# Kernel optimization log

Measured on AMD Instinct MI355X. Metric: run time of the kernel, lower is better.

The kernel has to match this reference:

```python
import jax, jax.numpy as jnp
from jax import lax
import numpy as np

B = 8192
NUM_CTX = 300; NUM_STN = 300; NUM_GPE = 20; NUM_GPI = 2; NUM_OUT = 20
FF_DIM = 20; FF_STEPS = 20; STN_ITERS = 50
ETA_GPE = 1.0; ETA_STN = 1.0 / 3.0; ETA_GPI = 0.1
A1 = 1.0; A2 = 1.0; THETAD1 = 0.0; THETAD2 = 0.0
UNITS = (64, 128, 64)

_SPECS = [("vf0", UNITS[0], NUM_CTX), ("vf1", UNITS[1], UNITS[0]), ("vf2", UNITS[2], UNITS[1]), ("vf3", 1, UNITS[2]),
          ("jd1", FF_DIM, NUM_CTX), ("jd2", FF_DIM, NUM_CTX), ("kd1", FF_DIM, NUM_CTX), ("kd2", FF_DIM, NUM_CTX),
          ("sg", NUM_GPE, NUM_STN), ("gs", NUM_STN, NUM_GPE), ("glat", NUM_GPE, NUM_GPE), ("slat", NUM_STN, NUM_STN),
          ("d1gpi", NUM_GPI, FF_DIM), ("stngpi", NUM_GPI, NUM_STN),
          ("ih", 4 * NUM_OUT, NUM_GPI), ("hh", 4 * NUM_OUT, NUM_OUT)]


def _lin_init(k, out_d, in_d):
    kw, kb = jax.random.split(k)
    bound = 1.0 / np.sqrt(in_d)
    w = jax.random.uniform(kw, (out_d, in_d), minval=-bound, maxval=bound, dtype=jnp.float32)
    b = jax.random.uniform(kb, (out_d,), minval=-bound, maxval=bound, dtype=jnp.float32)
    return w, b


def setup_inputs() -> dict:
    key = jax.random.key(0)
    ks = iter(jax.random.split(key, 40))
    inp = {}
    inp["stimulus"] = jax.random.normal(next(ks), (B, NUM_CTX), dtype=jnp.float32)
    inp["deltavf"] = jax.random.normal(next(ks), (B, 1), dtype=jnp.float32)
    inp["hx0"] = jax.random.uniform(next(ks), (B, NUM_OUT), dtype=jnp.float32)
    inp["cx0"] = jax.random.uniform(next(ks), (B, NUM_OUT), dtype=jnp.float32)
    for name, o, i in _SPECS:
        w, b = _lin_init(next(ks), o, i)
        inp["w_" + name] = w
        inp["b_" + name] = b
    return inp


def _lin(x, w, b):
    return x @ w.T + b


def _lstm_cell(x, h, c, w_ih, b_ih, w_hh, b_hh):
    gates = _lin(x, w_ih, b_ih) + _lin(h, w_hh, b_hh)
    i, f, g, o = jnp.split(gates, 4, axis=-1)  # torch LSTMCell gate order
    c_new = jax.nn.sigmoid(f) * c + jax.nn.sigmoid(i) * jnp.tanh(g)
    h_new = jax.nn.sigmoid(o) * jnp.tanh(c_new)
    return h_new, c_new


def reference(stimulus, deltavf, hx0, cx0,
              w_vf0, b_vf0, w_vf1, b_vf1, w_vf2, b_vf2, w_vf3, b_vf3,
              w_jd1, b_jd1, w_jd2, b_jd2, w_kd1, b_kd1, w_kd2, b_kd2,
              w_sg, b_sg, w_gs, b_gs, w_glat, b_glat, w_slat, b_slat,
              w_d1gpi, b_d1gpi, w_stngpi, b_stngpi,
              w_ih, b_ih, w_hh, b_hh):
    bsz = stimulus.shape[0]
    # value function head
    h = jax.nn.relu(_lin(stimulus, w_vf0, b_vf0))
    h = jax.nn.relu(_lin(h, w_vf1, b_vf1))
    h = jax.nn.relu(_lin(h, w_vf2, b_vf2))
    vt = jnp.tanh(_lin(h, w_vf3, b_vf3))  # [B, 1]

    lamd1 = jax.nn.sigmoid(A1 * (deltavf - THETAD1))  # [B, 1]
    lamd2 = jax.nn.sigmoid(A2 * (deltavf - THETAD2))  # [B, 1]

    # loop-invariant striatal drives (computed every iter in torch, same value)
    J_D1 = _lin(stimulus, w_jd1, b_jd1)
    J_D2 = _lin(stimulus, w_jd2, b_jd2)
    K_D1 = _lin(stimulus, w_kd1, b_kd1)
    K_D2 = _lin(stimulus, w_kd2, b_kd2)

    def ff_step(carry, _):
        v1, v2 = carry
        v1 = jax.nn.sigmoid(lamd1 * (J_D1 * (1.0 - v1) + (1.0 - K_D1) * v1))
        v2 = jax.nn.sigmoid(lamd2 * (J_D2 * (1.0 - v2) + (1.0 - K_D2) * v2))
        return (v1, v2), None

    z_ff = jnp.zeros((bsz, FF_DIM), dtype=stimulus.dtype)
    (V_D1, V_D2), _ = lax.scan(ff_step, (z_ff, z_ff), None, length=FF_STEPS)

    V_GPi_DP = _lin(V_D1, w_d1gpi, b_d1gpi)  # [B, num_gpi]

    def stn_step(carry, _):
        xgpe, xstn, vstn, vgpi, hx, cx = carry
        xgpe = xgpe + ETA_GPE * (-xgpe + _lin(vstn, w_sg, b_sg) + _lin(xgpe, w_glat, b_glat) - V_D2)
        xstn = xstn + ETA_STN * (-xstn + _lin(xgpe, w_gs, b_gs) + _lin(vstn, w_slat, b_slat))
        vstn = jnp.tanh(lamd2 * xstn)
        V_GPi_IP = lamd2 * _lin(vstn, w_stngpi, b_stngpi)
        vgpi = vgpi + ETA_GPI * (-vgpi - V_GPi_DP + 2.0 * V_GPi_IP)
        hx, cx = _lstm_cell(-vgpi, hx, cx, w_ih, b_ih, w_hh, b_hh)
        return (xgpe, xstn, vstn, vgpi, hx, cx), None

    carry0 = (jnp.zeros((bsz, NUM_GPE), dtype=stimulus.dtype),
              jnp.zeros((bsz, NUM_STN), dtype=stimulus.dtype),
              jnp.zeros((bsz, NUM_STN), dtype=stimulus.dtype),  # tanh(lamd2*0) = 0
              jnp.zeros((bsz, NUM_GPI), dtype=stimulus.dtype),
              hx0, cx0)
    carry, _ = lax.scan(stn_step, carry0, None, length=STN_ITERS)
    hx = carry[4]
    return hx, vt
```

## Files before the change

kernel.cpp:

```cpp
#include <hip/hip_runtime.h>


typedef _Float16 f16_t;
typedef _Float16 f16x8 __attribute__((ext_vector_type(8)));
typedef _Float16 f16x4 __attribute__((ext_vector_type(4)));
typedef float floatx4 __attribute__((ext_vector_type(4)));

#define BTOT 8192
#define BM   32
#define NTHR 512
#define NBLK 256
#define VSTR 328
#define XST  32

struct Params {
  const float *stimulus, *deltavf, *hx0, *cx0;
  const float *w_vf0, *b_vf0, *w_vf1, *b_vf1, *w_vf2, *b_vf2, *w_vf3, *b_vf3;
  const float *w_jd1, *b_jd1, *w_jd2, *b_jd2, *w_kd1, *b_kd1, *w_kd2, *b_kd2;
  const float *w_sg, *b_sg, *w_gs, *b_gs, *w_glat, *b_glat, *w_slat, *b_slat;
  const float *w_d1gpi, *b_d1gpi, *w_stngpi, *b_stngpi;
  const float *w_ih, *b_ih, *w_hh, *b_hh;
  float* out;
};

struct __align__(16) Smem {
  f16_t vstn[BM * VSTR];
  f16_t xgpe[2][BM * XST];
  f16_t hxf[BM * XST];
  f16_t wB2[21 * 512];
  f16_t wsp[10 * 512];
  f16_t whh[5 * 512];
  union { float h1f[BM * 128]; float scr[3200]; float gates[BM * 80]; } u;
  float h0f[BM * 64];
  float V_D2f[BM * 20];
  float bsumS[304];
  float bsg[20];
  float bihh[80], wih0[80], wih1[80];
  float DPs[BM * 2], vgpis[BM * 2], lamS[BM];
};

__device__ __forceinline__ float rcp_f(float x) { return __builtin_amdgcn_rcpf(x); }
__device__ __forceinline__ float sigm_fast(float x) { return rcp_f(1.f + __expf(-x)); }
__device__ __forceinline__ float tanh_fast(float x) { return 1.f - 2.f * rcp_f(1.f + __expf(2.f * x)); }

__device__ __forceinline__ f16x8 ldfrag(const float* row, int k0, int kmax, bool valid) {
  float4 z = make_float4(0.f, 0.f, 0.f, 0.f);
  int nv = valid ? (kmax - k0) : 0;
  float4 f0 = (nv >= 4) ? *(const float4*)(row + k0) : z;
  float4 f1 = (nv >= 8) ? *(const float4*)(row + k0 + 4) : z;
  f16x8 r;
  r[0] = (f16_t)f0.x; r[1] = (f16_t)f0.y; r[2] = (f16_t)f0.z; r[3] = (f16_t)f0.w;
  r[4] = (f16_t)f1.x; r[5] = (f16_t)f1.y; r[6] = (f16_t)f1.z; r[7] = (f16_t)f1.w;
  return r;
}

__global__ __launch_bounds__(NTHR, 2) void bg_main(Params P) {
  __shared__ Smem S;
  const int tid  = threadIdx.x;
  const int lane = tid & 63;
  const int wv   = tid >> 6;
  const int q    = lane >> 4;
  const int cl   = lane & 15;
  const int row0 = blockIdx.x * BM;
  const floatx4 zf = {0.f, 0.f, 0.f, 0.f};

  if (tid < BM) S.lamS[tid] = sigm_fast(P.deltavf[row0 + tid]);
  for (int i = tid; i < BM * 2; i += NTHR) S.vgpis[i] = 0.f;
  for (int i = tid; i < 2 * BM * XST; i += NTHR) ((f16_t*)S.xgpe)[i] = (f16_t)0.f;
  for (int i = tid; i < BM * XST; i += NTHR) {
    int m = i >> 5, j = i & 31;
    S.hxf[i] = (j < 20) ? (f16_t)P.hx0[row0 * 20 + m * 20 + j] : (f16_t)0.f;
  }
  for (int i = tid; i < BM * VSTR; i += NTHR) S.vstn[i] = (f16_t)0.f;
  for (int i = tid; i < 21 * 512; i += NTHR) {
    int t = i >> 9, l = (i >> 3) & 63, jj = i & 7;
    int c2 = l & 15, k = ((l >> 4) << 3) + jj;
    float v = 0.f;
    if (t < 19) { int n = t * 16 + c2; if (n < 300 && k < 20) v = P.w_gs[n * 20 + k]; }
    else        { int g = (t - 19) * 16 + c2; if (g < 20 && k < 20) v = P.w_glat[g * 20 + k]; }
    S.wB2[i] = (f16_t)v;
  }
  for (int i = tid; i < 10 * 512; i += NTHR) {
    int c = i >> 9, l = (i >> 3) & 63, jj = i & 7;
    int p = l & 15, k = c * 32 + ((l >> 4) << 3) + jj;
    float v = (p < 2 && k < 300) ? P.w_stngpi[p * 300 + k] : 0.f;
    S.wsp[i] = (f16_t)v;
  }
  for (int i = tid; i < 5 * 512; i += NTHR) {
    int t = i >> 9, l = (i >> 3) & 63, jj = i & 7;
    int g = t * 16 + (l & 15), k = ((l >> 4) << 3) + jj;
    S.whh[i] = (f16_t)((k < 20) ? P.w_hh[g * 20 + k] : 0.f);
  }
  for (int i = tid; i < 304; i += NTHR) S.bsumS[i] = (i < 300) ? (P.b_slat[i] + P.b_gs[i]) : 0.f;
  for (int i = tid; i < 20; i += NTHR)  S.bsg[i] = P.b_sg[i] + P.b_glat[i];
  for (int i = tid; i < 80; i += NTHR) {
    S.bihh[i] = P.b_ih[i] + P.b_hh[i];
    S.wih0[i] = P.w_ih[i * 2 + 0];
    S.wih1[i] = P.w_ih[i * 2 + 1];
  }

  {
    int o = tid & 63, mb = (tid >> 6) * 4;
    const float4* wr = (const float4*)(P.w_vf0 + o * 300);
    float bias = P.b_vf0[o], a[4];
#pragma unroll
    for (int u = 0; u < 4; ++u) a[u] = bias;
    for (int kq = 0; kq < 75; ++kq) {
      float4 w = wr[kq];
#pragma unroll
      for (int u = 0; u < 4; ++u) {
        float4 v = *(const float4*)(P.stimulus + (size_t)(row0 + mb + u) * 300 + kq * 4);
        a[u] = fmaf(v.x, w.x, a[u]); a[u] = fmaf(v.y, w.y, a[u]);
        a[u] = fmaf(v.z, w.z, a[u]); a[u] = fmaf(v.w, w.w, a[u]);
      }
    }
#pragma unroll
    for (int u = 0; u < 4; ++u) S.h0f[(mb + u) * 64 + o] = fmaxf(a[u], 0.f);
  }
  __syncthreads();
  {
    int o = tid & 127, mb = (tid >> 7) * 8;
    const float* wr = P.w_vf1 + o * 64;
    float bias = P.b_vf1[o], a[8];
#pragma unroll
    for (int u = 0; u < 8; ++u) a[u] = bias;
    for (int k = 0; k < 64; ++k) {
      float w = wr[k];
#pragma unroll
      for (int u = 0; u < 8; ++u) a[u] = fmaf(S.h0f[(mb + u) * 64 + k], w, a[u]);
    }
#pragma unroll
    for (int u = 0; u < 8; ++u) S.u.h1f[(mb + u) * 128 + o] = fmaxf(a[u], 0.f);
  }
  __syncthreads();
  {
    int o = tid & 63, mb = (tid >> 6) * 4;
    const float* wr = P.w_vf2 + o * 128;
    float bias = P.b_vf2[o], a[4];
#pragma unroll
    for (int u = 0; u < 4; ++u) a[u] = bias;
    for (int k = 0; k < 128; ++k) {
      float w = wr[k];
#pragma unroll
      for (int u = 0; u < 4; ++u) a[u] = fmaf(S.u.h1f[(mb + u) * 128 + k], w, a[u]);
    }
#pragma unroll
    for (int u = 0; u < 4; ++u) S.h0f[(mb + u) * 64 + o] = fmaxf(a[u], 0.f);
  }
  __syncthreads();
  {
    int oid = tid & 127, mb = (tid >> 7) * 8;
    if (oid < 80) {
      int which = oid / 20, o = oid - which * 20;
      const float *wp, *bp;
      if (which == 0)      { wp = P.w_jd1; bp = P.b_jd1; }
      else if (which == 1) { wp = P.w_jd2; bp = P.b_jd2; }
      else if (which == 2) { wp = P.w_kd1; bp = P.b_kd1; }
      else                 { wp = P.w_kd2; bp = P.b_kd2; }
      float bias = bp[o], a[8];
#pragma unroll
      for (int u = 0; u < 8; ++u) a[u] = bias;
      for (int kq = 0; kq < 75; ++kq) {
        float4 w = *(const float4*)(wp + o * 300 + kq * 4);
#pragma unroll
        for (int u = 0; u < 8; ++u) {
          float4 v = *(const float4*)(P.stimulus + (size_t)(row0 + mb + u) * 300 + kq * 4);
          a[u] = fmaf(v.x, w.x, a[u]); a[u] = fmaf(v.y, w.y, a[u]);
          a[u] = fmaf(v.z, w.z, a[u]); a[u] = fmaf(v.w, w.w, a[u]);
        }
      }
#pragma unroll
      for (int u = 0; u < 8; ++u) S.u.scr[which * 640 + (mb + u) * 20 + o] = a[u];
    }
    if (tid < BM) {
      float a = P.b_vf3[0];
      for (int k = 0; k < 64; ++k) a = fmaf(S.h0f[tid * 64 + k], P.w_vf3[k], a);
      P.out[(size_t)BTOT * 20 + row0 + tid] = tanh_fast(a);
    }
  }
  __syncthreads();
  for (int i = tid; i < BM * 20; i += NTHR) {
    int m = i / 20;
    float j1 = S.u.scr[i],        j2 = S.u.scr[640 + i];
    float k1 = S.u.scr[1280 + i], k2 = S.u.scr[1920 + i];
    float L = S.lamS[m], v1 = 0.f, v2 = 0.f;
    for (int s = 0; s < 20; ++s) {
      v1 = sigm_fast(L * (j1 * (1.f - v1) + (1.f - k1) * v1));
      v2 = sigm_fast(L * (j2 * (1.f - v2) + (1.f - k2) * v2));
    }
    S.u.scr[2560 + i] = v1;
    S.V_D2f[i] = v2;
  }
  __syncthreads();
  if (tid < BM * 2) {
    int m = tid >> 1, p2 = tid & 1;
    float a = P.b_d1gpi[p2];
    for (int o = 0; o < 20; ++o) a = fmaf(S.u.scr[2560 + m * 20 + o], P.w_d1gpi[p2 * 20 + o], a);
    S.DPs[tid] = a;
  }
  __syncthreads();

  f16x8 Ws[3][10];
#pragma unroll
  for (int j = 0; j < 3; ++j) {
    int t = wv + 8 * j;
    if (t < 19) {
      int n = t * 16 + cl;
#pragma unroll
      for (int c = 0; c < 10; ++c)
        Ws[j][c] = ldfrag(P.w_slat + (size_t)(n < 300 ? n : 0) * 300, c * 32 + q * 8, 300, n < 300);
    } else if (t < 21) {
      int g = (t - 19) * 16 + cl;
#pragma unroll
      for (int c = 0; c < 10; ++c)
        Ws[j][c] = ldfrag(P.w_sg + (size_t)(g < 20 ? g : 0) * 300, c * 32 + q * 8, 300, g < 20);
    } else {
      f16x8 z;
#pragma unroll
      for (int e = 0; e < 8; ++e) z[e] = (f16_t)0.f;
#pragma unroll
      for (int c = 0; c < 10; ++c) Ws[j][c] = z;
    }
  }
  const float lam0 = S.lamS[cl], lam1 = S.lamS[cl + 16];
  const float bstn0 = P.b_stngpi[0], bstn1 = P.b_stngpi[1];
  const int e0 = tid,        m0 = e0 / 20, j0 = e0 - m0 * 20;
  const int e1 = tid + NTHR, m1 = e1 / 20, j1 = e1 - m1 * 20;
  const bool hase1 = (tid < BM * 20 - NTHR);
  float cxr0 = P.cx0[row0 * 20 + e0], hxr0 = P.hx0[row0 * 20 + e0];
  float cxr1 = hase1 ? P.cx0[row0 * 20 + e1] : 0.f;
  float hxr1 = hase1 ? P.hx0[row0 * 20 + e1] : 0.f;

  float xs[3][2][4];
#pragma unroll
  for (int j = 0; j < 3; ++j)
#pragma unroll
    for (int mf = 0; mf < 2; ++mf)
#pragma unroll
      for (int r = 0; r < 4; ++r) xs[j][mf][r] = 0.f;

  for (int it = 0; it < 50; ++it) {
    const int po = it & 1, pn = po ^ 1;
    floatx4 acc[3][2];
#pragma unroll
    for (int j = 0; j < 3; ++j) { acc[j][0] = zf; acc[j][1] = zf; }

#pragma unroll
    for (int c = 0; c < 10; ++c) {
      f16x8 b0 = *(const f16x8*)&S.vstn[cl * VSTR + c * 32 + q * 8];
      f16x8 b1 = *(const f16x8*)&S.vstn[(16 + cl) * VSTR + c * 32 + q * 8];
#pragma unroll
      for (int j = 0; j < 3; ++j) {
        if (wv + 8 * j < 21) {
          acc[j][0] = __builtin_amdgcn_mfma_f32_16x16x32_f16(Ws[j][c], b0, acc[j][0], 0, 0, 0);
          acc[j][1] = __builtin_amdgcn_mfma_f32_16x16x32_f16(Ws[j][c], b1, acc[j][1], 0, 0, 0);
        }
      }
    }
    if (wv == 3 || wv == 4) {
      f16x8 Wg = *(const f16x8*)&S.wB2[(wv + 16) * 512 + lane * 8];
      f16x8 g0 = *(const f16x8*)&S.xgpe[po][cl * XST + q * 8];
      f16x8 g1 = *(const f16x8*)&S.xgpe[po][(16 + cl) * XST + q * 8];
      acc[2][0] = __builtin_amdgcn_mfma_f32_16x16x32_f16(Wg, g0, acc[2][0], 0, 0, 0);
      acc[2][1] = __builtin_amdgcn_mfma_f32_16x16x32_f16(Wg, g1, acc[2][1], 0, 0, 0);
      int g0i = (wv - 3) * 16 + q * 4;
      if (g0i < 20) {
        floatx4 bg4 = *(const floatx4*)&S.bsg[g0i];
#pragma unroll
        for (int mf = 0; mf < 2; ++mf) {
          int batch = cl + 16 * mf;
          floatx4 vd4 = *(const floatx4*)&S.V_D2f[batch * 20 + g0i];
          f16x4 pk;
#pragma unroll
          for (int r = 0; r < 4; ++r) pk[r] = (f16_t)(acc[2][mf][r] + bg4[r] - vd4[r]);
          *(f16x4*)&S.xgpe[pn][batch * XST + g0i] = pk;
        }
      }
    }
    __syncthreads();

    {
      f16x8 x0 = *(const f16x8*)&S.xgpe[pn][cl * XST + q * 8];
      f16x8 x1 = *(const f16x8*)&S.xgpe[pn][(16 + cl) * XST + q * 8];
#pragma unroll
      for (int j = 0; j < 3; ++j) {
        int t = wv + 8 * j;
        if (t < 19) {
          f16x8 Wg = *(const f16x8*)&S.wB2[t * 512 + lane * 8];
          acc[j][0] = __builtin_amdgcn_mfma_f32_16x16x32_f16(Wg, x0, acc[j][0], 0, 0, 0);
          acc[j][1] = __builtin_amdgcn_mfma_f32_16x16x32_f16(Wg, x1, acc[j][1], 0, 0, 0);
        }
      }
#pragma unroll
      for (int j = 0; j < 3; ++j) {
        int t = wv + 8 * j;
        if (t < 19) {
          int n0 = t * 16 + q * 4;
          if (!(t == 18 && q == 3)) {
            floatx4 bs4 = *(const floatx4*)&S.bsumS[n0];
#pragma unroll
            for (int mf = 0; mf < 2; ++mf) {
              float lm = mf ? lam1 : lam0;
              f16x4 pk;
#pragma unroll
              for (int r = 0; r < 4; ++r) {
                float xo = xs[j][mf][r];
                float xn = xo + (1.0f / 3.0f) * (acc[j][mf][r] + bs4[r] - xo);
                xs[j][mf][r] = xn;
                pk[r] = (f16_t)tanh_fast(lm * xn);
              }
              *(f16x4*)&S.vstn[(cl + 16 * mf) * VSTR + n0] = pk;
            }
          }
        }
      }
    }
    __syncthreads();

    if (wv == 5) {
      floatx4 ip0 = zf, ip1 = zf;
#pragma unroll
      for (int c = 0; c < 10; ++c) {
        f16x8 Wp = *(const f16x8*)&S.wsp[c * 512 + lane * 8];
        f16x8 b0 = *(const f16x8*)&S.vstn[cl * VSTR + c * 32 + q * 8];
        f16x8 b1 = *(const f16x8*)&S.vstn[(16 + cl) * VSTR + c * 32 + q * 8];
        ip0 = __builtin_amdgcn_mfma_f32_16x16x32_f16(Wp, b0, ip0, 0, 0, 0);
        ip1 = __builtin_amdgcn_mfma_f32_16x16x32_f16(Wp, b1, ip1, 0, 0, 0);
      }
      if (q == 0) {
#pragma unroll
        for (int mf = 0; mf < 2; ++mf) {
          int batch = cl + 16 * mf;
          float lm = mf ? lam1 : lam0;
#pragma unroll
          for (int p = 0; p < 2; ++p) {
            float raw = (mf ? ip1[p] : ip0[p]) + (p ? bstn1 : bstn0);
            float ipv = lm * raw;
            int idx = batch * 2 + p;
            float v = S.vgpis[idx];
            v = v + 0.1f * (-v - S.DPs[idx] + 2.f * ipv);
            S.vgpis[idx] = v;
          }
        }
      }
    } else if (wv < 5) {
      f16x8 Wh = *(const f16x8*)&S.whh[wv * 512 + lane * 8];
      f16x8 h0 = *(const f16x8*)&S.hxf[cl * XST + q * 8];
      f16x8 h1 = *(const f16x8*)&S.hxf[(16 + cl) * XST + q * 8];
      floatx4 gA = __builtin_amdgcn_mfma_f32_16x16x32_f16(Wh, h0, zf, 0, 0, 0);
      floatx4 gB = __builtin_amdgcn_mfma_f32_16x16x32_f16(Wh, h1, zf, 0, 0, 0);
      int gb = wv * 16 + q * 4;
      *(floatx4*)&S.u.gates[cl * 80 + gb] = gA;
      *(floatx4*)&S.u.gates[(cl + 16) * 80 + gb] = gB;
    }
    __syncthreads();

    {
      float v0 = S.vgpis[m0 * 2], v1 = S.vgpis[m0 * 2 + 1];
      float gi = S.u.gates[m0 * 80 + j0]      + S.bihh[j0]      - S.wih0[j0] * v0      - S.wih1[j0] * v1;
      float gf = S.u.gates[m0 * 80 + 20 + j0] + S.bihh[20 + j0] - S.wih0[20 + j0] * v0 - S.wih1[20 + j0] * v1;
      float gg = S.u.gates[m0 * 80 + 40 + j0] + S.bihh[40 + j0] - S.wih0[40 + j0] * v0 - S.wih1[40 + j0] * v1;
      float go = S.u.gates[m0 * 80 + 60 + j0] + S.bihh[60 + j0] - S.wih0[60 + j0] * v0 - S.wih1[60 + j0] * v1;
      float cn = sigm_fast(gf) * cxr0 + sigm_fast(gi) * tanh_fast(gg);
      cxr0 = cn;
      hxr0 = sigm_fast(go) * tanh_fast(cn);
      S.hxf[m0 * XST + j0] = (f16_t)hxr0;
    }
    if (hase1) {
      float v0 = S.vgpis[m1 * 2], v1 = S.vgpis[m1 * 2 + 1];
      float gi = S.u.gates[m1 * 80 + j1]      + S.bihh[j1]      - S.wih0[j1] * v0      - S.wih1[j1] * v1;
      float gf = S.u.gates[m1 * 80 + 20 + j1] + S.bihh[20 + j1] - S.wih0[20 + j1] * v0 - S.wih1[20 + j1] * v1;
      float gg = S.u.gates[m1 * 80 + 40 + j1] + S.bihh[40 + j1] - S.wih0[40 + j1] * v0 - S.wih1[40 + j1] * v1;
      float go = S.u.gates[m1 * 80 + 60 + j1] + S.bihh[60 + j1] - S.wih0[60 + j1] * v0 - S.wih1[60 + j1] * v1;
      float cn = sigm_fast(gf) * cxr1 + sigm_fast(gi) * tanh_fast(gg);
      cxr1 = cn;
      hxr1 = sigm_fast(go) * tanh_fast(cn);
      S.hxf[m1 * XST + j1] = (f16_t)hxr1;
    }
    __syncthreads();
  }

  P.out[(size_t)row0 * 20 + e0] = hxr0;
  if (hase1) P.out[(size_t)row0 * 20 + e1] = hxr1;
}

extern "C" void kernel_launch(void* const* d_in, const int* in_sizes, int n_in,
                              void* d_out, int out_size, void* d_ws, size_t ws_size,
                              hipStream_t stream) {
  (void)in_sizes; (void)n_in; (void)out_size; (void)d_ws; (void)ws_size;
  Params P;
  P.stimulus = (const float*)d_in[0];
  P.deltavf  = (const float*)d_in[1];
  P.hx0 = (const float*)d_in[2];
  P.cx0 = (const float*)d_in[3];
  P.w_vf0 = (const float*)d_in[4];  P.b_vf0 = (const float*)d_in[5];
  P.w_vf1 = (const float*)d_in[6];  P.b_vf1 = (const float*)d_in[7];
  P.w_vf2 = (const float*)d_in[8];  P.b_vf2 = (const float*)d_in[9];
  P.w_vf3 = (const float*)d_in[10]; P.b_vf3 = (const float*)d_in[11];
  P.w_jd1 = (const float*)d_in[12]; P.b_jd1 = (const float*)d_in[13];
  P.w_jd2 = (const float*)d_in[14]; P.b_jd2 = (const float*)d_in[15];
  P.w_kd1 = (const float*)d_in[16]; P.b_kd1 = (const float*)d_in[17];
  P.w_kd2 = (const float*)d_in[18]; P.b_kd2 = (const float*)d_in[19];
  P.w_sg  = (const float*)d_in[20]; P.b_sg  = (const float*)d_in[21];
  P.w_gs  = (const float*)d_in[22]; P.b_gs  = (const float*)d_in[23];
  P.w_glat= (const float*)d_in[24]; P.b_glat= (const float*)d_in[25];
  P.w_slat= (const float*)d_in[26]; P.b_slat= (const float*)d_in[27];
  P.w_d1gpi  = (const float*)d_in[28]; P.b_d1gpi  = (const float*)d_in[29];
  P.w_stngpi = (const float*)d_in[30]; P.b_stngpi = (const float*)d_in[31];
  P.w_ih = (const float*)d_in[32]; P.b_ih = (const float*)d_in[33];
  P.w_hh = (const float*)d_in[34]; P.b_hh = (const float*)d_in[35];
  P.out  = (float*)d_out;
  bg_main<<<NBLK, NTHR, 0, stream>>>(P);
}
```

Before: 410.5 us.

## Pipeline LSTM/GPi stage on dedicated wave with double-buffered vstn

Raises the block to 12 waves. 11 waves run the GPe/STN MFMA recurrence, and a 12th wave handles the GPi readout and LSTM gate update one iteration behind, reading a double-buffered vstn. This removes one of the three barriers per iteration and overlaps the LSTM work with the STN matmuls. It also spreads the STN tiles over more waves so each holds fewer weight registers. In exchange the single LSTM wave does serial work per iteration, and the larger block with 3-block launch bounds tightens the register budget.

```diff
diff --git a/kernel.cpp b/kernel.cpp
--- a/kernel.cpp
+++ b/kernel.cpp
@@ -8,7 +8,7 @@
 
 #define BTOT 8192
 #define BM   32
-#define NTHR 512
+#define NTHR 768
 #define NBLK 256
 #define VSTR 328
 #define XST  32
@@ -24,7 +24,7 @@
 };
 
 struct __align__(16) Smem {
-  f16_t vstn[BM * VSTR];
+  f16_t vstn[2][BM * VSTR];
   f16_t xgpe[2][BM * XST];
   f16_t hxf[BM * XST];
   f16_t wB2[21 * 512];
@@ -54,7 +54,7 @@
   return r;
 }
 
-__global__ __launch_bounds__(NTHR, 2) void bg_main(Params P) {
+__global__ __launch_bounds__(NTHR, 3) void bg_main(Params P) {
   __shared__ Smem S;
   const int tid  = threadIdx.x;
   const int lane = tid & 63;
@@ -66,12 +66,12 @@
 
   if (tid < BM) S.lamS[tid] = sigm_fast(P.deltavf[row0 + tid]);
   for (int i = tid; i < BM * 2; i += NTHR) S.vgpis[i] = 0.f;
+  for (int i = tid; i < 2 * BM * VSTR; i += NTHR) ((f16_t*)S.vstn)[i] = (f16_t)0.f;
   for (int i = tid; i < 2 * BM * XST; i += NTHR) ((f16_t*)S.xgpe)[i] = (f16_t)0.f;
   for (int i = tid; i < BM * XST; i += NTHR) {
     int m = i >> 5, j = i & 31;
     S.hxf[i] = (j < 20) ? (f16_t)P.hx0[row0 * 20 + m * 20 + j] : (f16_t)0.f;
   }
-  for (int i = tid; i < BM * VSTR; i += NTHR) S.vstn[i] = (f16_t)0.f;
   for (int i = tid; i < 21 * 512; i += NTHR) {
     int t = i >> 9, l = (i >> 3) & 63, jj = i & 7;
     int c2 = l & 15, k = ((l >> 4) << 3) + jj;
@@ -83,8 +83,7 @@
   for (int i = tid; i < 10 * 512; i += NTHR) {
     int c = i >> 9, l = (i >> 3) & 63, jj = i & 7;
     int p = l & 15, k = c * 32 + ((l >> 4) << 3) + jj;
-    float v = (p < 2 && k < 300) ? P.w_stngpi[p * 300 + k] : 0.f;
-    S.wsp[i] = (f16_t)v;
+    S.wsp[i] = (f16_t)((p < 2 && k < 300) ? P.w_stngpi[p * 300 + k] : 0.f);
   }
   for (int i = tid; i < 5 * 512; i += NTHR) {
     int t = i >> 9, l = (i >> 3) & 63, jj = i & 7;
@@ -99,7 +98,7 @@
     S.wih1[i] = P.w_ih[i * 2 + 1];
   }
 
-  {
+  if (tid < 512) {
     int o = tid & 63, mb = (tid >> 6) * 4;
     const float4* wr = (const float4*)(P.w_vf0 + o * 300);
     float bias = P.b_vf0[o], a[4];
@@ -118,7 +117,7 @@
     for (int u = 0; u < 4; ++u) S.h0f[(mb + u) * 64 + o] = fmaxf(a[u], 0.f);
   }
   __syncthreads();
-  {
+  if (tid < 512) {
     int o = tid & 127, mb = (tid >> 7) * 8;
     const float* wr = P.w_vf1 + o * 64;
     float bias = P.b_vf1[o], a[8];
@@ -133,7 +132,7 @@
     for (int u = 0; u < 8; ++u) S.u.h1f[(mb + u) * 128 + o] = fmaxf(a[u], 0.f);
   }
   __syncthreads();
-  {
+  if (tid < 512) {
     int o = tid & 63, mb = (tid >> 6) * 4;
     const float* wr = P.w_vf2 + o * 128;
     float bias = P.b_vf2[o], a[4];
@@ -148,7 +147,7 @@
     for (int u = 0; u < 4; ++u) S.h0f[(mb + u) * 64 + o] = fmaxf(a[u], 0.f);
   }
   __syncthreads();
-  {
+  if (tid < 512) {
     int oid = tid & 127, mb = (tid >> 7) * 8;
     if (oid < 80) {
       int which = oid / 20, o = oid - which * 20;
@@ -200,188 +199,203 @@
   }
   __syncthreads();
 
-  f16x8 Ws[3][10];
-#pragma unroll
-  for (int j = 0; j < 3; ++j) {
-    int t = wv + 8 * j;
-    if (t < 19) {
-      int n = t * 16 + cl;
+  f16x8 WsA[10], WsB[10];
+  const int tA = wv, tB = wv + 11;
+  if (wv < 11) {
+#pragma unroll
+    for (int c = 0; c < 10; ++c)
+      WsA[c] = ldfrag(P.w_slat + (size_t)(tA * 16 + cl) * 300, c * 32 + q * 8, 300, true);
+    if (wv <= 7) {
+      int n = tB * 16 + cl;
 #pragma unroll
       for (int c = 0; c < 10; ++c)
-        Ws[j][c] = ldfrag(P.w_slat + (size_t)(n < 300 ? n : 0) * 300, c * 32 + q * 8, 300, n < 300);
-    } else if (t < 21) {
-      int g = (t - 19) * 16 + cl;
+        WsB[c] = ldfrag(P.w_slat + (size_t)(n < 300 ? n : 0) * 300, c * 32 + q * 8, 300, n < 300);
+    } else if (wv <= 9) {
+      int g = (tB - 19) * 16 + cl;
 #pragma unroll
       for (int c = 0; c < 10; ++c)
-        Ws[j][c] = ldfrag(P.w_sg + (size_t)(g < 20 ? g : 0) * 300, c * 32 + q * 8, 300, g < 20);
-    } else {
-      f16x8 z;
-#pragma unroll
-      for (int e = 0; e < 8; ++e) z[e] = (f16_t)0.f;
-#pragma unroll
-      for (int c = 0; c < 10; ++c) Ws[j][c] = z;
-    }
-  }
-  const float lam0 = S.lamS[cl], lam1 = S.lamS[cl + 16];
+        WsB[c] = ldfrag(P.w_sg + (size_t)(g < 20 ? g : 0) * 300, c * 32 + q * 8, 300, g < 20);
+    }
+  }
   const float bstn0 = P.b_stngpi[0], bstn1 = P.b_stngpi[1];
-  const int e0 = tid,        m0 = e0 / 20, j0 = e0 - m0 * 20;
-  const int e1 = tid + NTHR, m1 = e1 / 20, j1 = e1 - m1 * 20;
-  const bool hase1 = (tid < BM * 20 - NTHR);
-  float cxr0 = P.cx0[row0 * 20 + e0], hxr0 = P.hx0[row0 * 20 + e0];
-  float cxr1 = hase1 ? P.cx0[row0 * 20 + e1] : 0.f;
-  float hxr1 = hase1 ? P.hx0[row0 * 20 + e1] : 0.f;
-
-  float xs[3][2][4];
-#pragma unroll
-  for (int j = 0; j < 3; ++j)
-#pragma unroll
-    for (int mf = 0; mf < 2; ++mf)
-#pragma unroll
-      for (int r = 0; r < 4; ++r) xs[j][mf][r] = 0.f;
+  float xsA[2][4], xsB[2][4];
+#pragma unroll
+  for (int mf = 0; mf < 2; ++mf)
+#pragma unroll
+    for (int r = 0; r < 4; ++r) { xsA[mf][r] = 0.f; xsB[mf][r] = 0.f; }
+
+  const int cm = lane >> 1, cj0 = (lane & 1) * 10;
+  float cxr[10], hxr[10];
+  if (wv == 11) {
+#pragma unroll
+    for (int u = 0; u < 10; ++u) {
+      cxr[u] = P.cx0[row0 * 20 + lane * 10 + u];
+      hxr[u] = P.hx0[row0 * 20 + lane * 10 + u];
+    }
+  }
+
+  auto consume1 = [&](int po_) {
+    floatx4 ip0 = zf, ip1 = zf;
+#pragma unroll
+    for (int c = 0; c < 10; ++c) {
+      f16x8 Wp = *(const f16x8*)&S.wsp[c * 512 + lane * 8];
+      f16x8 b0 = *(const f16x8*)&S.vstn[po_][cl * VSTR + c * 32 + q * 8];
+      f16x8 b1 = *(const f16x8*)&S.vstn[po_][(16 + cl) * VSTR + c * 32 + q * 8];
+      ip0 = __builtin_amdgcn_mfma_f32_16x16x32_f16(Wp, b0, ip0, 0, 0, 0);
+      ip1 = __builtin_amdgcn_mfma_f32_16x16x32_f16(Wp, b1, ip1, 0, 0, 0);
+    }
+    if (q == 0) {
+#pragma unroll
+      for (int mf = 0; mf < 2; ++mf) {
+        int batch = cl + 16 * mf;
+        float lm = S.lamS[batch];
+#pragma unroll
+        for (int p = 0; p < 2; ++p) {
+          float raw = (mf ? ip1[p] : ip0[p]) + (p ? bstn1 : bstn0);
+          int idx = batch * 2 + p;
+          float v = S.vgpis[idx];
+          v = v + 0.1f * (-v - S.DPs[idx] + 2.f * (lm * raw));
+          S.vgpis[idx] = v;
+        }
+      }
+    }
+    f16x8 h0 = *(const f16x8*)&S.hxf[cl * XST + q * 8];
+    f16x8 h1 = *(const f16x8*)&S.hxf[(16 + cl) * XST + q * 8];
+    float vA0 = S.vgpis[cl * 2], vA1 = S.vgpis[cl * 2 + 1];
+    float vB0 = S.vgpis[(cl + 16) * 2], vB1 = S.vgpis[(cl + 16) * 2 + 1];
+#pragma unroll
+    for (int gt = 0; gt < 5; ++gt) {
+      f16x8 Wh = *(const f16x8*)&S.whh[gt * 512 + lane * 8];
+      floatx4 gA = __builtin_amdgcn_mfma_f32_16x16x32_f16(Wh, h0, zf, 0, 0, 0);
+      floatx4 gB = __builtin_amdgcn_mfma_f32_16x16x32_f16(Wh, h1, zf, 0, 0, 0);
+      int gb = gt * 16 + q * 4;
+      floatx4 bi = *(const floatx4*)&S.bihh[gb];
+      floatx4 w0 = *(const floatx4*)&S.wih0[gb];
+      floatx4 w1 = *(const floatx4*)&S.wih1[gb];
+#pragma unroll
+      for (int r = 0; r < 4; ++r) {
+        gA[r] += bi[r] - w0[r] * vA0 - w1[r] * vA1;
+        gB[r] += bi[r] - w0[r] * vB0 - w1[r] * vB1;
+      }
+      *(floatx4*)&S.u.gates[cl * 80 + gb] = gA;
+      *(floatx4*)&S.u.gates[(cl + 16) * 80 + gb] = gB;
+    }
+  };
+  auto consume2 = [&]() {
+#pragma unroll
+    for (int u = 0; u < 10; ++u) {
+      int j = cj0 + u;
+      float gi = S.u.gates[cm * 80 + j];
+      float gf = S.u.gates[cm * 80 + 20 + j];
+      float gg = S.u.gates[cm * 80 + 40 + j];
+      float go = S.u.gates[cm * 80 + 60 + j];
+      float cn = sigm_fast(gf) * cxr[u] + sigm_fast(gi) * tanh_fast(gg);
+      cxr[u] = cn;
+      float hn = sigm_fast(go) * tanh_fast(cn);
+      hxr[u] = hn;
+      S.hxf[cm * XST + j] = (f16_t)hn;
+    }
+  };
 
   for (int it = 0; it < 50; ++it) {
     const int po = it & 1, pn = po ^ 1;
-    floatx4 acc[3][2];
-#pragma unroll
-    for (int j = 0; j < 3; ++j) { acc[j][0] = zf; acc[j][1] = zf; }
-
-#pragma unroll
-    for (int c = 0; c < 10; ++c) {
-      f16x8 b0 = *(const f16x8*)&S.vstn[cl * VSTR + c * 32 + q * 8];
-      f16x8 b1 = *(const f16x8*)&S.vstn[(16 + cl) * VSTR + c * 32 + q * 8];
-#pragma unroll
-      for (int j = 0; j < 3; ++j) {
-        if (wv + 8 * j < 21) {
-          acc[j][0] = __builtin_amdgcn_mfma_f32_16x16x32_f16(Ws[j][c], b0, acc[j][0], 0, 0, 0);
-          acc[j][1] = __builtin_amdgcn_mfma_f32_16x16x32_f16(Ws[j][c], b1, acc[j][1], 0, 0, 0);
-        }
-      }
-    }
-    if (wv == 3 || wv == 4) {
-      f16x8 Wg = *(const f16x8*)&S.wB2[(wv + 16) * 512 + lane * 8];
-      f16x8 g0 = *(const f16x8*)&S.xgpe[po][cl * XST + q * 8];
-      f16x8 g1 = *(const f16x8*)&S.xgpe[po][(16 + cl) * XST + q * 8];
-      acc[2][0] = __builtin_amdgcn_mfma_f32_16x16x32_f16(Wg, g0, acc[2][0], 0, 0, 0);
-      acc[2][1] = __builtin_amdgcn_mfma_f32_16x16x32_f16(Wg, g1, acc[2][1], 0, 0, 0);
-      int g0i = (wv - 3) * 16 + q * 4;
-      if (g0i < 20) {
-        floatx4 bg4 = *(const floatx4*)&S.bsg[g0i];
-#pragma unroll
-        for (int mf = 0; mf < 2; ++mf) {
-          int batch = cl + 16 * mf;
-          floatx4 vd4 = *(const floatx4*)&S.V_D2f[batch * 20 + g0i];
-          f16x4 pk;
-#pragma unroll
-          for (int r = 0; r < 4; ++r) pk[r] = (f16_t)(acc[2][mf][r] + bg4[r] - vd4[r]);
-          *(f16x4*)&S.xgpe[pn][batch * XST + g0i] = pk;
-        }
-      }
+    floatx4 aA[2], aB[2];
+    aA[0] = zf; aA[1] = zf; aB[0] = zf; aB[1] = zf;
+    if (wv < 11) {
+#pragma unroll
+      for (int c = 0; c < 10; ++c) {
+        f16x8 b0 = *(const f16x8*)&S.vstn[po][cl * VSTR + c * 32 + q * 8];
+        f16x8 b1 = *(const f16x8*)&S.vstn[po][(16 + cl) * VSTR + c * 32 + q * 8];
+        aA[0] = __builtin_amdgcn_mfma_f32_16x16x32_f16(WsA[c], b0, aA[0], 0, 0, 0);
+        aA[1] = __builtin_amdgcn_mfma_f32_16x16x32_f16(WsA[c], b1, aA[1], 0, 0, 0);
+        if (wv <= 9) {
+          aB[0] = __builtin_amdgcn_mfma_f32_16x16x32_f16(WsB[c], b0, aB[0], 0, 0, 0);
+          aB[1] = __builtin_amdgcn_mfma_f32_16x16x32_f16(WsB[c], b1, aB[1], 0, 0, 0);
+        }
+      }
+      if (wv == 8 || wv == 9) {
+        f16x8 Wg = *(const f16x8*)&S.wB2[tB * 512 + lane * 8];
+        f16x8 g0 = *(const f16x8*)&S.xgpe[po][cl * XST + q * 8];
+        f16x8 g1 = *(const f16x8*)&S.xgpe[po][(16 + cl) * XST + q * 8];
+        aB[0] = __builtin_amdgcn_mfma_f32_16x16x32_f16(Wg, g0, aB[0], 0, 0, 0);
+        aB[1] = __builtin_amdgcn_mfma_f32_16x16x32_f16(Wg, g1, aB[1], 0, 0, 0);
+        int g0i = (tB - 19) * 16 + q * 4;
+        if (g0i < 20) {
+          floatx4 bg4 = *(const floatx4*)&S.bsg[g0i];
+#pragma unroll
+          for (int mf = 0; mf < 2; ++mf) {
+            int batch = cl + 16 * mf;
+            floatx4 vd4 = *(const floatx4*)&S.V_D2f[batch * 20 + g0i];
+            f16x4 pk;
+#pragma unroll
+            for (int r = 0; r < 4; ++r) pk[r] = (f16_t)(aB[mf][r] + bg4[r] - vd4[r]);
+            *(f16x4*)&S.xgpe[pn][batch * XST + g0i] = pk;
+          }
+        }
+      }
+    } else if (it > 0) {
+      consume1(po);
     }
     __syncthreads();
 
-    {
+    if (wv < 11) {
       f16x8 x0 = *(const f16x8*)&S.xgpe[pn][cl * XST + q * 8];
       f16x8 x1 = *(const f16x8*)&S.xgpe[pn][(16 + cl) * XST + q * 8];
-#pragma unroll
-      for (int j = 0; j < 3; ++j) {
-        int t = wv + 8 * j;
-        if (t < 19) {
-          f16x8 Wg = *(const f16x8*)&S.wB2[t * 512 + lane * 8];
-          acc[j][0] = __builtin_amdgcn_mfma_f32_16x16x32_f16(Wg, x0, acc[j][0], 0, 0, 0);
-          acc[j][1] = __builtin_amdgcn_mfma_f32_16x16x32_f16(Wg, x1, acc[j][1], 0, 0, 0);
-        }
-      }
-#pragma unroll
-      for (int j = 0; j < 3; ++j) {
-        int t = wv + 8 * j;
-        if (t < 19) {
-          int n0 = t * 16 + q * 4;
-          if (!(t == 18 && q == 3)) {
-            floatx4 bs4 = *(const floatx4*)&S.bsumS[n0];
-#pragma unroll
-            for (int mf = 0; mf < 2; ++mf) {
-              float lm = mf ? lam1 : lam0;
-              f16x4 pk;
-#pragma unroll
-              for (int r = 0; r < 4; ++r) {
-                float xo = xs[j][mf][r];
-                float xn = xo + (1.0f / 3.0f) * (acc[j][mf][r] + bs4[r] - xo);
-                xs[j][mf][r] = xn;
-                pk[r] = (f16_t)tanh_fast(lm * xn);
-              }
-              *(f16x4*)&S.vstn[(cl + 16 * mf) * VSTR + n0] = pk;
+      {
+        f16x8 Wg = *(const f16x8*)&S.wB2[tA * 512 + lane * 8];
+        aA[0] = __builtin_amdgcn_mfma_f32_16x16x32_f16(Wg, x0, aA[0], 0, 0, 0);
+        aA[1] = __builtin_amdgcn_mfma_f32_16x16x32_f16(Wg, x1, aA[1], 0, 0, 0);
+        int n0 = tA * 16 + q * 4;
+        floatx4 bs4 = *(const floatx4*)&S.bsumS[n0];
+#pragma unroll
+        for (int mf = 0; mf < 2; ++mf) {
+          float lm = S.lamS[cl + 16 * mf];
+          f16x4 pk;
+#pragma unroll
+          for (int r = 0; r < 4; ++r) {
+            float xo = xsA[mf][r];
+            float xn = xo + (1.0f / 3.0f) * (aA[mf][r] + bs4[r] - xo);
+            xsA[mf][r] = xn;
+            pk[r] = (f16_t)tanh_fast(lm * xn);
+          }
+          *(f16x4*)&S.vstn[pn][(cl + 16 * mf) * VSTR + n0] = pk;
+        }
+      }
+      if (wv <= 7) {
+        f16x8 Wg = *(const f16x8*)&S.wB2[tB * 512 + lane * 8];
+        aB[0] = __builtin_amdgcn_mfma_f32_16x16x32_f16(Wg, x0, aB[0], 0, 0, 0);
+        aB[1] = __builtin_amdgcn_mfma_f32_16x16x32_f16(Wg, x1, aB[1], 0, 0, 0);
+        int n0 = tB * 16 + q * 4;
+        if (!(tB == 18 && q == 3)) {
+          floatx4 bs4 = *(const floatx4*)&S.bsumS[n0];
+#pragma unroll
+          for (int mf = 0; mf < 2; ++mf) {
+            float lm = S.lamS[cl + 16 * mf];
+            f16x4 pk;
+#pragma unroll
+            for (int r = 0; r < 4; ++r) {
+              float xo = xsB[mf][r];
+              float xn = xo + (1.0f / 3.0f) * (aB[mf][r] + bs4[r] - xo);
+              xsB[mf][r] = xn;
+              pk[r] = (f16_t)tanh_fast(lm * xn);
             }
+            *(f16x4*)&S.vstn[pn][(cl + 16 * mf) * VSTR + n0] = pk;
           }
         }
       }
+    } else if (it > 0) {
+      consume2();
     }
     __syncthreads();
-
-    if (wv == 5) {
-      floatx4 ip0 = zf, ip1 = zf;
-#pragma unroll
-      for (int c = 0; c < 10; ++c) {
-        f16x8 Wp = *(const f16x8*)&S.wsp[c * 512 + lane * 8];
-        f16x8 b0 = *(const f16x8*)&S.vstn[cl * VSTR + c * 32 + q * 8];
-        f16x8 b1 = *(const f16x8*)&S.vstn[(16 + cl) * VSTR + c * 32 + q * 8];
-        ip0 = __builtin_amdgcn_mfma_f32_16x16x32_f16(Wp, b0, ip0, 0, 0, 0);
-        ip1 = __builtin_amdgcn_mfma_f32_16x16x32_f16(Wp, b1, ip1, 0, 0, 0);
-      }
-      if (q == 0) {
-#pragma unroll
-        for (int mf = 0; mf < 2; ++mf) {
-          int batch = cl + 16 * mf;
-          float lm = mf ? lam1 : lam0;
-#pragma unroll
-          for (int p = 0; p < 2; ++p) {
-            float raw = (mf ? ip1[p] : ip0[p]) + (p ? bstn1 : bstn0);
-            float ipv = lm * raw;
-            int idx = batch * 2 + p;
-            float v = S.vgpis[idx];
-            v = v + 0.1f * (-v - S.DPs[idx] + 2.f * ipv);
-            S.vgpis[idx] = v;
-          }
-        }
-      }
-    } else if (wv < 5) {
-      f16x8 Wh = *(const f16x8*)&S.whh[wv * 512 + lane * 8];
-      f16x8 h0 = *(const f16x8*)&S.hxf[cl * XST + q * 8];
-      f16x8 h1 = *(const f16x8*)&S.hxf[(16 + cl) * XST + q * 8];
-      floatx4 gA = __builtin_amdgcn_mfma_f32_16x16x32_f16(Wh, h0, zf, 0, 0, 0);
-      floatx4 gB = __builtin_amdgcn_mfma_f32_16x16x32_f16(Wh, h1, zf, 0, 0, 0);
-      int gb = wv * 16 + q * 4;
-      *(floatx4*)&S.u.gates[cl * 80 + gb] = gA;
-      *(floatx4*)&S.u.gates[(cl + 16) * 80 + gb] = gB;
-    }
-    __syncthreads();
-
-    {
-      float v0 = S.vgpis[m0 * 2], v1 = S.vgpis[m0 * 2 + 1];
-      float gi = S.u.gates[m0 * 80 + j0]      + S.bihh[j0]      - S.wih0[j0] * v0      - S.wih1[j0] * v1;
-      float gf = S.u.gates[m0 * 80 + 20 + j0] + S.bihh[20 + j0] - S.wih0[20 + j0] * v0 - S.wih1[20 + j0] * v1;
-      float gg = S.u.gates[m0 * 80 + 40 + j0] + S.bihh[40 + j0] - S.wih0[40 + j0] * v0 - S.wih1[40 + j0] * v1;
-      float go = S.u.gates[m0 * 80 + 60 + j0] + S.bihh[60 + j0] - S.wih0[60 + j0] * v0 - S.wih1[60 + j0] * v1;
-      float cn = sigm_fast(gf) * cxr0 + sigm_fast(gi) * tanh_fast(gg);
-      cxr0 = cn;
-      hxr0 = sigm_fast(go) * tanh_fast(cn);
-      S.hxf[m0 * XST + j0] = (f16_t)hxr0;
-    }
-    if (hase1) {
-      float v0 = S.vgpis[m1 * 2], v1 = S.vgpis[m1 * 2 + 1];
-      float gi = S.u.gates[m1 * 80 + j1]      + S.bihh[j1]      - S.wih0[j1] * v0      - S.wih1[j1] * v1;
-      float gf = S.u.gates[m1 * 80 + 20 + j1] + S.bihh[20 + j1] - S.wih0[20 + j1] * v0 - S.wih1[20 + j1] * v1;
-      float gg = S.u.gates[m1 * 80 + 40 + j1] + S.bihh[40 + j1] - S.wih0[40 + j1] * v0 - S.wih1[40 + j1] * v1;
-      float go = S.u.gates[m1 * 80 + 60 + j1] + S.bihh[60 + j1] - S.wih0[60 + j1] * v0 - S.wih1[60 + j1] * v1;
-      float cn = sigm_fast(gf) * cxr1 + sigm_fast(gi) * tanh_fast(gg);
-      cxr1 = cn;
-      hxr1 = sigm_fast(go) * tanh_fast(cn);
-      S.hxf[m1 * XST + j1] = (f16_t)hxr1;
-    }
-    __syncthreads();
-  }
-
-  P.out[(size_t)row0 * 20 + e0] = hxr0;
-  if (hase1) P.out[(size_t)row0 * 20 + e1] = hxr1;
+  }
+
+  if (wv == 11) {
+    consume1(0);
+    consume2();
+#pragma unroll
+    for (int u = 0; u < 10; ++u)
+      P.out[(size_t)row0 * 20 + lane * 10 + u] = hxr[u];
+  }
 }
 
 extern "C" void kernel_launch(void* const* d_in, const int* in_sizes, int n_in,
```

New measurement: 436.0 us. 6.2% more time.
